# Kernel optimization log

Measured on AMD Instinct MI355X. Metric: run time of the kernel, lower is better.

The kernel has to match this reference:

```python
import jax, jax.numpy as jnp
from jax import lax
import numpy as np

S, WL, V, E, OC, H = 512, 100, 50000, 200, 50, 400  # sents, words, vocab, emb, conv out-ch, hidden


def setup_inputs() -> dict:
    key = jax.random.key(0)
    ks = jax.random.split(key, 40)
    lengths = jax.random.randint(ks[0], (S,), 20, WL + 1)
    tok = jax.random.randint(ks[1], (S, WL), 1, V)
    x = jnp.where(jnp.arange(WL)[None, :] < lengths[:, None], tok, 0)  # 0 = pad

    def p(i, shape):
        return jax.random.normal(ks[i], shape, jnp.float32) * 0.05

    inp = {"x": x, "num_of_sent": 3, "emb": p(2, (V, E))}
    for K in range(8):
        inp[f"conv_w{K}"] = p(3 + K, (OC, E, 2 * K + 1))
    inp["conv_b"] = p(11, (8, OC))
    names = ["w_ih_f", "w_hh_f", "b_ih_f", "b_hh_f", "w_ih_b", "w_hh_b", "b_ih_b", "b_hh_b"]
    shapes = [(3 * H, H), (3 * H, H), (3 * H,), (3 * H,)] * 2
    for j, (n, s) in enumerate(zip(names, shapes)):
        inp[n] = p(12 + j, s)
    inp["W_doc"] = p(20, (H, 2 * H)); inp["b_doc"] = p(21, (H,))
    inp["W_d1"] = p(22, (100, 4 * H)); inp["b_d1"] = p(23, (100,))
    inp["W_d2"] = p(24, (1, 100)); inp["b_d2"] = p(25, (1,))
    inp["W_r"] = p(26, (H, 2 * H)); inp["b_r"] = p(27, (H,))
    return inp


def _gru_dir(xs, w_ih, w_hh, b_ih, b_hh, reverse):
    gi = xs @ w_ih.T + b_ih  # [S, 3H] input projections precomputed

    def step(h, gi_t):
        gh = w_hh @ h + b_hh
        r = jax.nn.sigmoid(gi_t[:H] + gh[:H])
        z = jax.nn.sigmoid(gi_t[H:2 * H] + gh[H:2 * H])
        n = jnp.tanh(gi_t[2 * H:] + r * gh[2 * H:])
        h_new = (1.0 - z) * n + z * h
        return h_new, h_new

    return lax.scan(step, jnp.zeros(H, xs.dtype), gi, reverse=reverse)[1]


def _forward(x, num_of_sent, emb, conv_ws, conv_b, gru_f, gru_b,
             W_doc, b_doc, W_d1, b_d1, W_d2, b_d2, W_r, b_r):
    lengths = (x > 0).sum(axis=1)  # sum(sign(x), dim=1)
    wf = emb[x]                            # [S, WL, E]
    ci = jnp.swapaxes(wf, 1, 2)            # [S, E, WL]
    dn = ('NCH', 'OIH', 'NCH')
    feats = [lax.conv_general_dilated(ci, w, (1,), 'SAME', dimension_numbers=dn)
             + conv_b[k][None, :, None] for k, w in enumerate(conv_ws)]
    sf = jnp.swapaxes(jnp.concatenate(feats, axis=1), 1, 2)  # [S, WL, 400]
    mask = (jnp.arange(WL)[None, :] < lengths[:, None]).astype(sf.dtype)
    pooled = (sf * mask[:, :, None]).sum(axis=1) / lengths[:, None].astype(sf.dtype)  # ragged avg-pool [S,400]
    hf = _gru_dir(pooled, *gru_f, reverse=False)
    hb = _gru_dir(pooled, *gru_b, reverse=True)
    enc = jnp.concatenate([hf, hb], axis=1)  # [S, 800]
    doc = jnp.tanh(W_doc @ enc.mean(axis=0) + b_doc)  # [400]

    def dec_step(carry, enc_i):
        g, count = carry
        feat = jnp.concatenate([enc_i, g, doc])  # [1600]
        p = jax.nn.sigmoid(W_d2 @ jnp.tanh(W_d1 @ feat + b_d1) + b_d2)[0]
        allowed = jnp.logical_or(num_of_sent <= 0, count < num_of_sent)
        sel = jnp.logical_and(allowed, p > 0.5)  # greedy decision
        g = g + sel.astype(g.dtype) * jnp.tanh(W_r @ enc_i + b_r)
        count = count + sel.astype(count.dtype)
        term = jnp.where(sel, p, 1.0 - p)
        return (g, count), (term, sel)

    init = (jnp.zeros(H, enc.dtype), jnp.zeros((), jnp.int32))
    _, (terms, sels) = lax.scan(dec_step, init, enc)
    logp = jnp.log(terms * 0.99999 + 5e-6).sum()
    return logp, sels.astype(jnp.int32)


def reference(x, num_of_sent, emb, conv_w0, conv_w1, conv_w2, conv_w3, conv_w4, conv_w5, conv_w6, conv_w7,
              conv_b, w_ih_f, w_hh_f, b_ih_f, b_hh_f, w_ih_b, w_hh_b, b_ih_b, b_hh_b,
              W_doc, b_doc, W_d1, b_d1, W_d2, b_d2, W_r, b_r):
    conv_ws = (conv_w0, conv_w1, conv_w2, conv_w3, conv_w4, conv_w5, conv_w6, conv_w7)
    gru_f = (w_ih_f, w_hh_f, b_ih_f, b_hh_f)
    gru_b = (w_ih_b, w_hh_b, b_ih_b, b_hh_b)
    return _forward(x, num_of_sent, emb, conv_ws, conv_b, gru_f, gru_b,
                    W_doc, b_doc, W_d1, b_d1, W_d2, b_d2, W_r, b_r)
```

## Files before the change

### kernel.cpp

```cpp
#include <hip/hip_runtime.h>
#include <math.h>

#define S_N   512
#define WL_N  100
#define E_N   200
#define OC_N  50
#define H_N   400

template<int K>
__device__ inline float conv_dot(const float* __restrict__ wbase,
                                 const float (*Ap)[17], int lane)
{
  constexpr int W = 2 * K + 1;
  constexpr int n = E_N * W;
  float acc = 0.f;
  for (int idx = lane; idx < n; idx += 64) {
    int e = idx / W;
    int k = idx - e * W;
    acc += wbase[idx] * Ap[e][7 - K + k];
  }
  return acc;
}

__global__ __launch_bounds__(256, 1)
void pooled_kernel(const int* __restrict__ x, const float* __restrict__ emb,
                   const float* __restrict__ cw0, const float* __restrict__ cw1,
                   const float* __restrict__ cw2, const float* __restrict__ cw3,
                   const float* __restrict__ cw4, const float* __restrict__ cw5,
                   const float* __restrict__ cw6, const float* __restrict__ cw7,
                   const float* __restrict__ conv_b, float* __restrict__ pooled)
{
  const int s = blockIdx.x;
  const int tid = threadIdx.x;
  __shared__ int xr[WL_N];
  __shared__ int Lsh;
  __shared__ float Apart[E_N][17];
  __shared__ float Bpart[E_N][9];
  if (tid < WL_N) xr[tid] = x[s * WL_N + tid];
  __syncthreads();
  if (tid == 0) {
    int L = 0;
    for (int t = 0; t < WL_N; ++t) L += (xr[t] != 0) ? 1 : 0;
    Lsh = L;
  }
  __syncthreads();
  const int L = Lsh;
  const int Lp7 = (L + 7 < WL_N) ? (L + 7) : WL_N;
  if (tid < E_N) {
    const int e = tid;
    float acc = 0.f;
    for (int t = 0; t < Lp7; ++t) {
      acc += emb[(size_t)xr[t] * E_N + e];
      int m = t + 1;
      if (m <= 7) Bpart[e][m] = acc;
      int rel = m - (L - 7);
      if (rel >= 0 && rel < 15) Apart[e][rel] = acc;
    }
    const float accF = acc;
    #pragma unroll
    for (int dd = 0; dd < 15; ++dd) {
      int m = L - 7 + dd;
      float A = (m > WL_N) ? accF : Apart[e][dd];
      int d = dd - 7;
      float B = (d > 0) ? Bpart[e][d] : 0.f;
      Apart[e][dd] = A - B;
    }
  }
  __syncthreads();
  const float invL = 1.f / (float)L;
  const int wv = tid >> 6, lane = tid & 63;
  for (int p = wv; p < 400; p += 4) {
    const int K = p / 50, oc = p % 50;
    float acc = 0.f;
    switch (K) {
      case 0: acc = conv_dot<0>(cw0 + (size_t)oc * 200,  Apart, lane); break;
      case 1: acc = conv_dot<1>(cw1 + (size_t)oc * 600,  Apart, lane); break;
      case 2: acc = conv_dot<2>(cw2 + (size_t)oc * 1000, Apart, lane); break;
      case 3: acc = conv_dot<3>(cw3 + (size_t)oc * 1400, Apart, lane); break;
      case 4: acc = conv_dot<4>(cw4 + (size_t)oc * 1800, Apart, lane); break;
      case 5: acc = conv_dot<5>(cw5 + (size_t)oc * 2200, Apart, lane); break;
      case 6: acc = conv_dot<6>(cw6 + (size_t)oc * 2600, Apart, lane); break;
      case 7: acc = conv_dot<7>(cw7 + (size_t)oc * 3000, Apart, lane); break;
    }
    acc += __shfl_xor(acc, 1);  acc += __shfl_xor(acc, 2);
    acc += __shfl_xor(acc, 4);  acc += __shfl_xor(acc, 8);
    acc += __shfl_xor(acc, 16); acc += __shfl_xor(acc, 32);
    if (lane == 0)
      pooled[(size_t)s * 400 + p] = conv_b[p] + acc * invL;
  }
}

__global__ __launch_bounds__(256, 2)
void gemm_gi(const float* __restrict__ A,
             const float* __restrict__ wf, const float* __restrict__ bf,
             const float* __restrict__ wb, const float* __restrict__ bb,
             float* __restrict__ C)
{
  __shared__ float As[16][65];
  __shared__ float Bs[16][65];
  const int bm = blockIdx.y * 64, bn = blockIdx.x * 64;
  const int tid = threadIdx.x;
  const int tr = (tid / 16) * 4, tc = (tid % 16) * 4;
  float acc[4][4] = {};
  for (int k0 = 0; k0 < 400; k0 += 16) {
    for (int l = tid; l < 64 * 16; l += 256) {
      int r = l / 16, c = l % 16;
      As[c][r] = A[(size_t)(bm + r) * 400 + k0 + c];
    }
    for (int l = tid; l < 64 * 16; l += 256) {
      int r = l / 16, c = l % 16;
      int gcol = bn + r;
      float v = 0.f;
      if (gcol < 1200)      v = wf[(size_t)gcol * 400 + k0 + c];
      else if (gcol < 2400) v = wb[(size_t)(gcol - 1200) * 400 + k0 + c];
      Bs[c][r] = v;
    }
    __syncthreads();
    #pragma unroll
    for (int kk = 0; kk < 16; ++kk) {
      float a[4], b[4];
      #pragma unroll
      for (int u = 0; u < 4; ++u) { a[u] = As[kk][tr + u]; b[u] = Bs[kk][tc + u]; }
      #pragma unroll
      for (int u = 0; u < 4; ++u)
        #pragma unroll
        for (int v = 0; v < 4; ++v) acc[u][v] += a[u] * b[v];
    }
    __syncthreads();
  }
  for (int u = 0; u < 4; ++u) {
    int r = bm + tr + u;
    for (int v = 0; v < 4; ++v) {
      int c = bn + tc + v; if (c >= 2400) continue;
      float bias = (c < 1200) ? bf[c] : bb[c - 1200];
      C[(size_t)r * 2400 + c] = acc[u][v] + bias;
    }
  }
}

template<int TAG>
__global__ __launch_bounds__(256, 4)
void gemm32(const float* __restrict__ A, int lda,
            const float* __restrict__ Bw, int ldb,
            const float* __restrict__ bias,
            float* __restrict__ C, int ldc,
            int M, int N, int K, int act)
{
  __shared__ float As[32][33];
  __shared__ float Bs[32][33];
  const int bm = blockIdx.y * 32, bn = blockIdx.x * 32;
  const int tid = threadIdx.x;
  const int tr = (tid >> 4) * 2, tc = (tid & 15) * 2;
  float acc[2][2] = {};
  for (int k0 = 0; k0 < K; k0 += 32) {
    #pragma unroll
    for (int p = 0; p < 4; ++p) {
      int l = tid + p * 256;
      int r = l >> 5, c = l & 31;
      As[c][r] = (bm + r < M) ? A[(size_t)(bm + r) * lda + k0 + c] : 0.f;
      Bs[c][r] = (bn + r < N) ? Bw[(size_t)(bn + r) * ldb + k0 + c] : 0.f;
    }
    __syncthreads();
    #pragma unroll
    for (int kk = 0; kk < 32; ++kk) {
      float a0 = As[kk][tr], a1 = As[kk][tr + 1];
      float b0 = Bs[kk][tc], b1 = Bs[kk][tc + 1];
      acc[0][0] += a0 * b0; acc[0][1] += a0 * b1;
      acc[1][0] += a1 * b0; acc[1][1] += a1 * b1;
    }
    __syncthreads();
  }
  #pragma unroll
  for (int u = 0; u < 2; ++u) {
    int r = bm + tr + u; if (r >= M) continue;
    #pragma unroll
    for (int v = 0; v < 2; ++v) {
      int c = bn + tc + v; if (c >= N) continue;
      float xv = acc[u][v] + (bias ? bias[c] : 0.f);
      if (act == 1) xv = tanhf(xv);
      C[(size_t)r * ldc + c] = xv;
    }
  }
}

#define GRU_NB 25
#define GRU_CHUNK 16
#define LDA64(p) __hip_atomic_load((p), __ATOMIC_RELAXED, __HIP_MEMORY_SCOPE_AGENT)
__global__ __launch_bounds__(256, 1)
void gru_scan_kernel(const float* __restrict__ gi,
                     const float* __restrict__ whh_f, const float* __restrict__ bhh_f,
                     const float* __restrict__ whh_b, const float* __restrict__ bhh_b,
                     float* __restrict__ enc,
                     float* __restrict__ mean,
                     unsigned long long* __restrict__ hbuf)
{
  const int tid = threadIdx.x;
  const int dir = blockIdx.x / GRU_NB;
  const int b   = blockIdx.x % GRU_NB;
  const float* whh = dir ? whh_b : whh_f;
  const float* bhh = dir ? bhh_b : bhh_f;
  unsigned long long* hb = hbuf + (size_t)dir * 800;
  const int i0 = b * GRU_CHUNK;

  __shared__ float wl[48][400];
  __shared__ float hs[400];
  __shared__ float ghs[48];

  for (int l = tid; l < 48 * 400; l += 256) {
    int lr = l / 400, c = l % 400;
    int g = lr / GRU_CHUNK, ii = lr % GRU_CHUNK;
    wl[lr][c] = whh[(size_t)(g * 400 + i0 + ii) * 400 + c];
  }

  const int i  = tid >> 4;
  const int cc = tid & 15;
  const int c0 = cc * 25;

  float blr = 0.f, blz = 0.f, bln = 0.f, msum = 0.f;
  float g0r = 0.f, g0z = 0.f, g0n = 0.f;
  float g1r = 0.f, g1z = 0.f, g1n = 0.f;
  if (tid < GRU_CHUNK) {
    blr = bhh[i0 + tid];
    blz = bhh[400 + i0 + tid];
    bln = bhh[800 + i0 + tid];
    {
      int t0 = dir ? 511 : 0;
      const float* g = gi + (size_t)t0 * 2400 + dir * 1200 + i0 + tid;
      g0r = g[0]; g0z = g[400]; g0n = g[800];
      int t1 = dir ? 510 : 1;
      g = gi + (size_t)t1 * 2400 + dir * 1200 + i0 + tid;
      g1r = g[0]; g1z = g[400]; g1n = g[800];
    }
  }
  __syncthreads();

  const int p = tid - 64;
  const bool h2 = (p >= 0) && (p < 16);

  for (int t = 0; t < 512; ++t) {
    const int t_in = dir ? (511 - t) : t;
    if (tid >= 64) {
      const unsigned long long* src = hb + (t & 1) * 400;
      const unsigned want = (unsigned)t;
      unsigned long long a0, a1, a2 = 0, b0, b1, b2 = 0, r0, r1, r2 = 0;
      a0 = LDA64(src + p); a1 = LDA64(src + p + 192); if (h2) a2 = LDA64(src + p + 384);
      b0 = LDA64(src + p); b1 = LDA64(src + p + 192); if (h2) b2 = LDA64(src + p + 384);
      for (;;) {
        bool ok = ((unsigned)(a0 >> 32) == want) && ((unsigned)(a1 >> 32) == want)
                  && (!h2 || ((unsigned)(a2 >> 32) == want));
        if (__all(ok)) { r0 = a0; r1 = a1; r2 = a2; break; }
        a0 = LDA64(src + p); a1 = LDA64(src + p + 192); if (h2) a2 = LDA64(src + p + 384);
        ok = ((unsigned)(b0 >> 32) == want) && ((unsigned)(b1 >> 32) == want)
             && (!h2 || ((unsigned)(b2 >> 32) == want));
        if (__all(ok)) { r0 = b0; r1 = b1; r2 = b2; break; }
        b0 = LDA64(src + p); b1 = LDA64(src + p + 192); if (h2) b2 = LDA64(src + p + 384);
      }
      hs[p] = __uint_as_float((unsigned)r0);
      hs[p + 192] = __uint_as_float((unsigned)r1);
      if (h2) hs[p + 384] = __uint_as_float((unsigned)r2);
    }
    __syncthreads();

    float a0 = 0.f, a1 = 0.f, a2 = 0.f;
    #pragma unroll
    for (int j = 0; j < 25; ++j) {
      float hv = hs[c0 + j];
      a0 += wl[i][c0 + j] * hv;
      a1 += wl[16 + i][c0 + j] * hv;
      a2 += wl[32 + i][c0 + j] * hv;
    }
    #pragma unroll
    for (int m = 1; m <= 8; m <<= 1) {
      a0 += __shfl_xor(a0, m);
      a1 += __shfl_xor(a1, m);
      a2 += __shfl_xor(a2, m);
    }
    if (cc == 0) { ghs[i] = a0; ghs[16 + i] = a1; ghs[32 + i] = a2; }
    __syncthreads();

    if (tid < GRU_CHUNK) {
      float r = 1.f / (1.f + expf(-(g0r + ghs[tid] + blr)));
      float z = 1.f / (1.f + expf(-(g0z + ghs[16 + tid] + blz)));
      float n = tanhf(g0n + r * (ghs[32 + tid] + bln));
      float hprev = hs[i0 + tid];
      float hn = (1.f - z) * n + z * hprev;
      msum += hn;
      unsigned long long pk =
          ((unsigned long long)(unsigned)(t + 1) << 32) |
          (unsigned long long)__float_as_uint(hn);
      __hip_atomic_store(hb + ((t + 1) & 1) * 400 + i0 + tid, pk,
                         __ATOMIC_RELAXED, __HIP_MEMORY_SCOPE_AGENT);
      enc[(size_t)t_in * 800 + dir * 400 + i0 + tid] = hn;
      g0r = g1r; g0z = g1z; g0n = g1n;
      int t2 = t + 2; if (t2 > 511) t2 = 511;
      int tn2 = dir ? (511 - t2) : t2;
      const float* g = gi + (size_t)tn2 * 2400 + dir * 1200 + i0 + tid;
      g1r = g[0]; g1z = g[400]; g1n = g[800];
    }
  }
  if (tid < GRU_CHUNK)
    mean[dir * 400 + i0 + tid] = msum * (1.f / 512.f);
}

__global__ void doc_kernel(const float* __restrict__ W_doc, const float* __restrict__ b_doc,
                           const float* __restrict__ mean, float* __restrict__ doc)
{
  int r = blockIdx.x, lane = threadIdx.x;
  float s = 0.f;
  for (int k = lane; k < 800; k += 64) s += W_doc[(size_t)r * 800 + k] * mean[k];
  s += __shfl_xor(s, 1);  s += __shfl_xor(s, 2);  s += __shfl_xor(s, 4);
  s += __shfl_xor(s, 8);  s += __shfl_xor(s, 16); s += __shfl_xor(s, 32);
  if (lane == 0) doc[r] = tanhf(s + b_doc[r]);
}

__global__ void docterm_kernel(const float* __restrict__ W_d1, const float* __restrict__ b_d1,
                               const float* __restrict__ doc, float* __restrict__ docterm)
{
  int r = blockIdx.x, lane = threadIdx.x;
  float s = 0.f;
  for (int k = lane; k < 400; k += 64) s += W_d1[(size_t)r * 1600 + 1200 + k] * doc[k];
  s += __shfl_xor(s, 1);  s += __shfl_xor(s, 2);  s += __shfl_xor(s, 4);
  s += __shfl_xor(s, 8);  s += __shfl_xor(s, 16); s += __shfl_xor(s, 32);
  if (lane == 0) docterm[r] = s + b_d1[r];
}

__global__ __launch_bounds__(1024, 1)
void decoder_kernel(const float* __restrict__ pre1,
                    const float* __restrict__ Qb,
                    const float* __restrict__ W_d2,
                    const float* __restrict__ b_d2,
                    const int* __restrict__ nos_p,
                    float* __restrict__ out)
{
  const int tid = threadIdx.x;
  const int row = tid >> 1;
  const int half = tid & 1;
  __shared__ float q[100];
  __shared__ float w2s[100];
  __shared__ int   selfl[512];
  __shared__ int   firstpos;
  __shared__ float red[16];
  if (tid < 100) { q[tid] = 0.f; w2s[tid] = W_d2[tid]; }
  if (tid < 512) selfl[tid] = 0;
  float pr[50];
  #pragma unroll
  for (int k = 0; k < 50; ++k) pr[k] = pre1[(size_t)row * 100 + half * 50 + k];
  const float bd2 = b_d2[0];
  const int nos = nos_p[0];
  int count = 0, seg = 0;
  float logp_part = 0.f;
  __syncthreads();

  for (int pass = 0; pass < 600 && seg < 512; ++pass) {
    const bool allowed = (nos <= 0) || (count < nos);
    if (tid == 0) firstpos = 512;
    float acc = 0.f;
    #pragma unroll
    for (int k = 0; k < 50; ++k)
      acc += w2s[half * 50 + k] * tanhf(pr[k] + q[half * 50 + k]);
    acc += __shfl_xor(acc, 1);
    const float sv = acc + bd2;
    __syncthreads();
    if (allowed && half == 0 && row >= seg && sv > 0.f)
      atomicMin(&firstpos, row);
    __syncthreads();
    const int fp = allowed ? firstpos : 512;
    const int lim = (fp < 512) ? fp : 511;
    if (half == 0 && row >= seg && row <= lim) {
      float p = 1.f / (1.f + expf(-sv));
      float term = (row == fp) ? p : (1.f - p);
      logp_part += logf(term * 0.99999f + 5e-6f);
      if (row == fp) selfl[row] = 1;
    }
    if (fp < 512) {
      if (tid < 100) q[tid] += Qb[(size_t)fp * 100 + tid];
      count += 1;
      seg = fp + 1;
    } else {
      seg = 512;
    }
    __syncthreads();
  }

  float v = logp_part;
  v += __shfl_xor(v, 1);  v += __shfl_xor(v, 2);  v += __shfl_xor(v, 4);
  v += __shfl_xor(v, 8);  v += __shfl_xor(v, 16); v += __shfl_xor(v, 32);
  if ((tid & 63) == 0) red[tid >> 6] = v;
  __syncthreads();
  if (tid == 0) {
    float s = 0.f;
    #pragma unroll
    for (int w = 0; w < 16; ++w) s += red[w];
    out[0] = s;
  }
  if (half == 0) out[1 + row] = (float)selfl[row];
}

extern "C" void kernel_launch(void* const* d_in, const int* in_sizes, int n_in,
                              void* d_out, int out_size, void* d_ws, size_t ws_size,
                              hipStream_t stream) {
  const int*   x      = (const int*)  d_in[0];
  const int*   nos    = (const int*)  d_in[1];
  const float* emb    = (const float*)d_in[2];
  const float* cw[8];
  for (int k = 0; k < 8; ++k) cw[k] = (const float*)d_in[3 + k];
  const float* conv_b = (const float*)d_in[11];
  const float* w_ih_f = (const float*)d_in[12];
  const float* w_hh_f = (const float*)d_in[13];
  const float* b_ih_f = (const float*)d_in[14];
  const float* b_hh_f = (const float*)d_in[15];
  const float* w_ih_b = (const float*)d_in[16];
  const float* w_hh_b = (const float*)d_in[17];
  const float* b_ih_b = (const float*)d_in[18];
  const float* b_hh_b = (const float*)d_in[19];
  const float* W_doc  = (const float*)d_in[20];
  const float* b_doc  = (const float*)d_in[21];
  const float* W_d1   = (const float*)d_in[22];
  const float* b_d1   = (const float*)d_in[23];
  const float* W_d2   = (const float*)d_in[24];
  const float* b_d2   = (const float*)d_in[25];
  const float* W_r    = (const float*)d_in[26];
  const float* b_r    = (const float*)d_in[27];

  float* ws = (float*)d_ws;
  const size_t OFF_POOLED  = 0;
  const size_t OFF_GI      = 204800;
  const size_t OFF_ENC     = 1433600;
  const size_t OFF_R       = 1843200;
  const size_t OFF_PRE1    = 2048000;
  const size_t OFF_MEAN    = 2099200;
  const size_t OFF_DOC     = 2100000;
  const size_t OFF_DOCTERM = 2100400;
  float* pooled  = ws + OFF_POOLED;
  float* gi      = ws + OFF_GI;
  float* enc     = ws + OFF_ENC;
  float* Rbuf    = ws + OFF_R;
  float* pre1    = ws + OFF_PRE1;
  float* mean    = ws + OFF_MEAN;
  float* doc     = ws + OFF_DOC;
  float* docterm = ws + OFF_DOCTERM;
  float* Qbuf    = ws + OFF_GI;
  unsigned long long* hbuf = (unsigned long long*)(ws + OFF_POOLED);

  pooled_kernel<<<512, 256, 0, stream>>>(x, emb, cw[0], cw[1], cw[2], cw[3],
                                         cw[4], cw[5], cw[6], cw[7], conv_b, pooled);

  gemm_gi<<<dim3(38, 8), 256, 0, stream>>>(pooled, w_ih_f, b_ih_f, w_ih_b, b_ih_b, gi);

  hipMemsetAsync(hbuf, 0, 1600 * sizeof(unsigned long long), stream);

  gru_scan_kernel<<<2 * GRU_NB, 256, 0, stream>>>(gi, w_hh_f, b_hh_f, w_hh_b, b_hh_b,
                                                  enc, mean, hbuf);

  doc_kernel<<<400, 64, 0, stream>>>(W_doc, b_doc, mean, doc);
  docterm_kernel<<<100, 64, 0, stream>>>(W_d1, b_d1, doc, docterm);

  gemm32<1><<<dim3(13, 16), 256, 0, stream>>>(enc, 800, W_r, 800, b_r,
                                              Rbuf, 400, 512, 400, 800, 1);
  gemm32<2><<<dim3(4, 16), 256, 0, stream>>>(Rbuf, 400, W_d1 + 800, 1600, nullptr,
                                             Qbuf, 100, 512, 100, 400, 0);
  gemm32<3><<<dim3(4, 16), 256, 0, stream>>>(enc, 800, W_d1, 1600, docterm,
                                             pre1, 100, 512, 100, 800, 0);

  decoder_kernel<<<1, 1024, 0, stream>>>(pre1, Qbuf, W_d2, b_d2, nos,
                                         (float*)d_out);
}
```

Before: 2.078 ms.

## Fuse post-GRU kernels: merge R/Q GEMMs, fold doc/docterm into decoder, drop memset

```diff
diff --git a/kernel.cpp b/kernel.cpp
--- a/kernel.cpp
+++ b/kernel.cpp
@@ -28,7 +28,8 @@
                    const float* __restrict__ cw2, const float* __restrict__ cw3,
                    const float* __restrict__ cw4, const float* __restrict__ cw5,
                    const float* __restrict__ cw6, const float* __restrict__ cw7,
-                   const float* __restrict__ conv_b, float* __restrict__ pooled)
+                   const float* __restrict__ conv_b, float* __restrict__ pooled,
+                   unsigned long long* __restrict__ hz)
 {
   const int s = blockIdx.x;
   const int tid = threadIdx.x;
@@ -36,6 +37,8 @@
   __shared__ int Lsh;
   __shared__ float Apart[E_N][17];
   __shared__ float Bpart[E_N][9];
+  if (blockIdx.x == 0)
+    for (int l = tid; l < 1600; l += 256) hz[l] = 0ull;
   if (tid < WL_N) xr[tid] = x[s * WL_N + tid];
   __syncthreads();
   if (tid == 0) {
@@ -180,6 +183,49 @@
       if (act == 1) xv = tanhf(xv);
       C[(size_t)r * ldc + c] = xv;
     }
+  }
+}
+
+__global__ __launch_bounds__(256, 2)
+void rq_kernel(const float* __restrict__ enc,
+               const float* __restrict__ W_r,
+               const float* __restrict__ b_r,
+               const float* __restrict__ W_d1,
+               float* __restrict__ Q)
+{
+  __shared__ float es[8][800];
+  __shared__ float Rt[8][401];
+  const int r0 = blockIdx.x * 8;
+  const int tid = threadIdx.x;
+  for (int l = tid; l < 6400; l += 256) {
+    int rr = l / 800, c = l % 800;
+    es[rr][c] = enc[(size_t)(r0 + rr) * 800 + c];
+  }
+  __syncthreads();
+  const int r = tid >> 5;
+  const int l32 = tid & 31;
+  for (int c = l32; c < 400; c += 32) {
+    const float4* wr = (const float4*)(W_r + (size_t)c * 800);
+    float acc = 0.f;
+    #pragma unroll 4
+    for (int k4 = 0; k4 < 200; ++k4) {
+      float4 w = wr[k4];
+      const float* e = &es[r][k4 * 4];
+      acc += w.x * e[0] + w.y * e[1] + w.z * e[2] + w.w * e[3];
+    }
+    Rt[r][c] = tanhf(acc + b_r[c]);
+  }
+  __syncthreads();
+  for (int m = l32; m < 100; m += 32) {
+    const float4* wm = (const float4*)(W_d1 + (size_t)m * 1600 + 800);
+    float acc = 0.f;
+    #pragma unroll 4
+    for (int k4 = 0; k4 < 100; ++k4) {
+      float4 w = wm[k4];
+      const float* rv = &Rt[r][k4 * 4];
+      acc += w.x * rv[0] + w.y * rv[1] + w.z * rv[2] + w.w * rv[3];
+    }
+    Q[(size_t)(r0 + r) * 100 + m] = acc;
   }
 }
 
@@ -302,31 +348,13 @@
     mean[dir * 400 + i0 + tid] = msum * (1.f / 512.f);
 }
 
-__global__ void doc_kernel(const float* __restrict__ W_doc, const float* __restrict__ b_doc,
-                           const float* __restrict__ mean, float* __restrict__ doc)
-{
-  int r = blockIdx.x, lane = threadIdx.x;
-  float s = 0.f;
-  for (int k = lane; k < 800; k += 64) s += W_doc[(size_t)r * 800 + k] * mean[k];
-  s += __shfl_xor(s, 1);  s += __shfl_xor(s, 2);  s += __shfl_xor(s, 4);
-  s += __shfl_xor(s, 8);  s += __shfl_xor(s, 16); s += __shfl_xor(s, 32);
-  if (lane == 0) doc[r] = tanhf(s + b_doc[r]);
-}
-
-__global__ void docterm_kernel(const float* __restrict__ W_d1, const float* __restrict__ b_d1,
-                               const float* __restrict__ doc, float* __restrict__ docterm)
-{
-  int r = blockIdx.x, lane = threadIdx.x;
-  float s = 0.f;
-  for (int k = lane; k < 400; k += 64) s += W_d1[(size_t)r * 1600 + 1200 + k] * doc[k];
-  s += __shfl_xor(s, 1);  s += __shfl_xor(s, 2);  s += __shfl_xor(s, 4);
-  s += __shfl_xor(s, 8);  s += __shfl_xor(s, 16); s += __shfl_xor(s, 32);
-  if (lane == 0) docterm[r] = s + b_d1[r];
-}
-
 __global__ __launch_bounds__(1024, 1)
 void decoder_kernel(const float* __restrict__ pre1,
                     const float* __restrict__ Qb,
+                    const float* __restrict__ mean,
+                    const float* __restrict__ W_doc,
+                    const float* __restrict__ b_doc,
+                    const float* __restrict__ W_d1,
                     const float* __restrict__ W_d2,
                     const float* __restrict__ b_d2,
                     const int* __restrict__ nos_p,
@@ -335,16 +363,43 @@
   const int tid = threadIdx.x;
   const int row = tid >> 1;
   const int half = tid & 1;
+  __shared__ float mean_s[800];
+  __shared__ float doc_s[400];
+  __shared__ float dt_s[100];
   __shared__ float q[100];
   __shared__ float w2s[100];
   __shared__ int   selfl[512];
   __shared__ int   firstpos;
   __shared__ float red[16];
+
+  if (tid < 800) mean_s[tid] = mean[tid];
   if (tid < 100) { q[tid] = 0.f; w2s[tid] = W_d2[tid]; }
   if (tid < 512) selfl[tid] = 0;
+  __syncthreads();
+
+  const int w = tid >> 6, l = tid & 63;
+  for (int rr = 0; rr < 25; ++rr) {
+    int r = w * 25 + rr;
+    float s = 0.f;
+    for (int k = l; k < 800; k += 64) s += W_doc[(size_t)r * 800 + k] * mean_s[k];
+    s += __shfl_xor(s, 1);  s += __shfl_xor(s, 2);  s += __shfl_xor(s, 4);
+    s += __shfl_xor(s, 8);  s += __shfl_xor(s, 16); s += __shfl_xor(s, 32);
+    if (l == 0) doc_s[r] = tanhf(s + b_doc[r]);
+  }
+  __syncthreads();
+  for (int r = w; r < 100; r += 16) {
+    float s = 0.f;
+    for (int k = l; k < 400; k += 64) s += W_d1[(size_t)r * 1600 + 1200 + k] * doc_s[k];
+    s += __shfl_xor(s, 1);  s += __shfl_xor(s, 2);  s += __shfl_xor(s, 4);
+    s += __shfl_xor(s, 8);  s += __shfl_xor(s, 16); s += __shfl_xor(s, 32);
+    if (l == 0) dt_s[r] = s;
+  }
+  __syncthreads();
+
   float pr[50];
   #pragma unroll
-  for (int k = 0; k < 50; ++k) pr[k] = pre1[(size_t)row * 100 + half * 50 + k];
+  for (int k = 0; k < 50; ++k)
+    pr[k] = pre1[(size_t)row * 100 + half * 50 + k] + dt_s[half * 50 + k];
   const float bd2 = b_d2[0];
   const int nos = nos_p[0];
   int count = 0, seg = 0;
@@ -390,7 +445,7 @@
   if (tid == 0) {
     float s = 0.f;
     #pragma unroll
-    for (int w = 0; w < 16; ++w) s += red[w];
+    for (int ww = 0; ww < 16; ++ww) s += red[ww];
     out[0] = s;
   }
   if (half == 0) out[1 + row] = (float)selfl[row];
@@ -426,42 +481,31 @@
   const size_t OFF_POOLED  = 0;
   const size_t OFF_GI      = 204800;
   const size_t OFF_ENC     = 1433600;
-  const size_t OFF_R       = 1843200;
+  const size_t OFF_HBUF    = 1843200;
   const size_t OFF_PRE1    = 2048000;
   const size_t OFF_MEAN    = 2099200;
-  const size_t OFF_DOC     = 2100000;
-  const size_t OFF_DOCTERM = 2100400;
   float* pooled  = ws + OFF_POOLED;
   float* gi      = ws + OFF_GI;
   float* enc     = ws + OFF_ENC;
-  float* Rbuf    = ws + OFF_R;
   float* pre1    = ws + OFF_PRE1;
   float* mean    = ws + OFF_MEAN;
-  float* doc     = ws + OFF_DOC;
-  float* docterm = ws + OFF_DOCTERM;
   float* Qbuf    = ws + OFF_GI;
-  unsigned long long* hbuf = (unsigned long long*)(ws + OFF_POOLED);
+  unsigned long long* hbuf = (unsigned long long*)(ws + OFF_HBUF);
 
   pooled_kernel<<<512, 256, 0, stream>>>(x, emb, cw[0], cw[1], cw[2], cw[3],
-                                         cw[4], cw[5], cw[6], cw[7], conv_b, pooled);
+                                         cw[4], cw[5], cw[6], cw[7], conv_b,
+                                         pooled, hbuf);
 
   gemm_gi<<<dim3(38, 8), 256, 0, stream>>>(pooled, w_ih_f, b_ih_f, w_ih_b, b_ih_b, gi);
-
-  hipMemsetAsync(hbuf, 0, 1600 * sizeof(unsigned long long), stream);
 
   gru_scan_kernel<<<2 * GRU_NB, 256, 0, stream>>>(gi, w_hh_f, b_hh_f, w_hh_b, b_hh_b,
                                                   enc, mean, hbuf);
 
-  doc_kernel<<<400, 64, 0, stream>>>(W_doc, b_doc, mean, doc);
-  docterm_kernel<<<100, 64, 0, stream>>>(W_d1, b_d1, doc, docterm);
-
-  gemm32<1><<<dim3(13, 16), 256, 0, stream>>>(enc, 800, W_r, 800, b_r,
-                                              Rbuf, 400, 512, 400, 800, 1);
-  gemm32<2><<<dim3(4, 16), 256, 0, stream>>>(Rbuf, 400, W_d1 + 800, 1600, nullptr,
-                                             Qbuf, 100, 512, 100, 400, 0);
-  gemm32<3><<<dim3(4, 16), 256, 0, stream>>>(enc, 800, W_d1, 1600, docterm,
+  rq_kernel<<<64, 256, 0, stream>>>(enc, W_r, b_r, W_d1, Qbuf);
+
+  gemm32<3><<<dim3(4, 16), 256, 0, stream>>>(enc, 800, W_d1, 1600, b_d1,
                                              pre1, 100, 512, 100, 800, 0);
 
-  decoder_kernel<<<1, 1024, 0, stream>>>(pre1, Qbuf, W_d2, b_d2, nos,
-                                         (float*)d_out);
-}
+  decoder_kernel<<<1, 1024, 0, stream>>>(pre1, Qbuf, mean, W_doc, b_doc, W_d1,
+                                         W_d2, b_d2, nos, (float*)d_out);
+}
```

Measured after the change: 2.399 ms. 1.15x slower.
